# Kernel optimization log

Measured on AMD Instinct MI355X. Metric: run time of the kernel, lower is better.

The kernel has to match this reference:

```python
import jax, jax.numpy as jnp
import numpy as np

B, LQ, LK, D = 2, 2048, 2048, 1024
H, DK, DV = 16, 64, 64
EPS = 1e-6


def setup_inputs() -> dict:
    key = jax.random.key(0)
    ks = jax.random.split(key, 12)
    s = 1.0 / np.sqrt(D)
    return {
        "PE_states": jax.random.normal(ks[0], (B, LK, D), jnp.float32),
        "global_state": jax.random.normal(ks[1], (B, LQ, D), jnp.float32),
        "PE_statements": jax.random.normal(ks[2], (B, LK, D), jnp.float32),
        "PE_operators": jax.random.normal(ks[3], (B, LK, D), jnp.float32),
        "PE_solution_scores": jax.random.uniform(ks[4], (B, LK), jnp.float32),
        "mask": jax.random.randint(ks[5], (B, LQ, LK), 0, 2, jnp.int32),
        "w_q": jax.random.normal(ks[6], (D, H * DK), jnp.float32) * s,
        "w_k": jax.random.normal(ks[7], (D, H * DK), jnp.float32) * s,
        "w_v": jax.random.normal(ks[8], (D, H * DV), jnp.float32) * s,
        "w_fc": jax.random.normal(ks[9], (H * DV, D), jnp.float32) * s,
        "ln_gamma": jnp.ones((D,), jnp.float32),
        "ln_beta": jnp.zeros((D,), jnp.float32),
    }


def _layer_norm(x, gamma, beta):
    mu = jnp.mean(x, axis=-1, keepdims=True)
    var = jnp.mean(jnp.square(x - mu), axis=-1, keepdims=True)
    return (x - mu) * jax.lax.rsqrt(var + EPS) * gamma + beta


def reference(PE_states, global_state, PE_statements, PE_operators,
              PE_solution_scores, mask, w_q, w_k, w_v, w_fc, ln_gamma, ln_beta):
    # att_type == 'ca_sc', query_mode == 'PE', dropout == 0
    residual = global_state  # [B, LQ, D]
    q = (global_state @ w_q).reshape(B, LQ, H, DK).transpose(0, 2, 1, 3)   # bhqd
    k = (PE_states @ w_k).reshape(B, LK, H, DK).transpose(0, 2, 1, 3)      # bhkd
    v_s = (PE_statements @ w_v).reshape(B, LK, H, DV).transpose(0, 2, 1, 3)
    v_o = (PE_operators @ w_v).reshape(B, LK, H, DV).transpose(0, 2, 1, 3)

    temp = jnp.asarray(DK, jnp.float32) ** 0.5
    attn = jnp.einsum('bhqd,bhkd->bhqk', q / temp, k)  # [B,H,LQ,LK]
    # PE_solution_scores: per-key bias broadcast over heads and queries
    attn = (attn + PE_solution_scores[:, None, None, :]) / 2.0
    attn = jnp.where(mask[:, None, :, :] == 0, jnp.float32(-1e9), attn)
    attn = jax.nn.softmax(attn, axis=-1)

    def head_out(v):
        o = jnp.einsum('bhqk,bhkd->bhqd', attn, v)
        o = o.transpose(0, 2, 1, 3).reshape(B, LQ, H * DV)
        o = o @ w_fc + residual
        return _layer_norm(o, ln_gamma, ln_beta)

    statement_pred = head_out(v_s)
    operator_pred = head_out(v_o)
    return statement_pred, operator_pred
```

## Files before the change

### kernel.cpp

```cpp
#include <hip/hip_runtime.h>


typedef unsigned short u16;
typedef unsigned int   u32;
typedef unsigned long long u64;

typedef __attribute__((ext_vector_type(8))) short frag_ab;
typedef __attribute__((ext_vector_type(4))) float frag_cd;
typedef __attribute__((ext_vector_type(16))) float f32x16;
typedef __attribute__((ext_vector_type(8))) unsigned short u16x8;
typedef __attribute__((ext_vector_type(4))) unsigned short u16x4;
typedef __attribute__((ext_vector_type(2))) unsigned int u32x2;
typedef __attribute__((ext_vector_type(4))) int int4v;

__device__ __forceinline__ u16 f2bf(float f) {
    u32 x = __builtin_bit_cast(u32, f);
    return (u16)((x + 0x7fffu + ((x >> 16) & 1u)) >> 16);
}

__device__ __forceinline__ u32 pkbf(float a, float b) {
    return __builtin_amdgcn_perm(__builtin_bit_cast(u32, b),
                                 __builtin_bit_cast(u32, a), 0x07060302u);
}

#define GLDS16(gsrc, ldst)                                                     \
    __builtin_amdgcn_global_load_lds(                                          \
        (const __attribute__((address_space(1))) void*)(gsrc),                 \
        (__attribute__((address_space(3))) void*)(ldst), 16, 0, 0)

#define MFMA32(a, b, c) __builtin_amdgcn_mfma_f32_32x32x16_bf16(a, b, c, 0, 0, 0)

__global__ __launch_bounds__(256) void prep_kernel(
    const float* __restrict__ in0, const float* __restrict__ in1,
    const float* __restrict__ in2, const float* __restrict__ in3,
    u16* __restrict__ Ab4,
    const float* __restrict__ w_q, const float* __restrict__ w_k,
    const float* __restrict__ w_v, const float* __restrict__ w_fc,
    u16* __restrict__ wqT, u16* __restrict__ wkT,
    u16* __restrict__ wvT, u16* __restrict__ wfcT,
    const int* __restrict__ mask, u64* __restrict__ bits)
{
    __shared__ u16 tile[32][33];
    const int bid = blockIdx.x;
    const int tid = threadIdx.x;
    if (bid < 8192) {
        int z = bid >> 11;
        const float* in = z == 0 ? in0 : z == 1 ? in1 : z == 2 ? in2 : in3;
        u16* o = Ab4 + (size_t)z * 4194304;
        size_t i = ((size_t)(bid & 2047) * 256 + tid) * 8;
        float4 f0 = *(const float4*)(in + i);
        float4 f1 = *(const float4*)(in + i + 4);
        u16x8 t;
        t[0] = f2bf(f0.x); t[1] = f2bf(f0.y); t[2] = f2bf(f0.z); t[3] = f2bf(f0.w);
        t[4] = f2bf(f1.x); t[5] = f2bf(f1.y); t[6] = f2bf(f1.z); t[7] = f2bf(f1.w);
        *(u16x8*)(o + i) = t;
    } else if (bid < 12288) {
        int t = bid - 8192;
        int z = t >> 10;
        const float* in = z == 0 ? w_q : z == 1 ? w_k : z == 2 ? w_v : w_fc;
        u16* out = z == 0 ? wqT : z == 1 ? wkT : z == 2 ? wvT : wfcT;
        int bx = (t & 31) * 32, by = ((t >> 5) & 31) * 32;
        int tx = tid & 31, ty = tid >> 5;
        for (int i = 0; i < 32; i += 8)
            tile[ty + i][tx] = f2bf(in[(size_t)(by + ty + i) * 1024 + bx + tx]);
        __syncthreads();
        for (int i = 0; i < 32; i += 8)
            out[(size_t)(bx + ty + i) * 1024 + by + tx] = tile[tx][ty + i];
    } else {
        int pb = bid - 12288;
        int wv = tid >> 6, ln = tid & 63;
        long long base = (long long)pb * 2048 + wv * 512;
        for (int j = 0; j < 8; j++) {
            int v = mask[base + j * 64 + ln];
            u64 bl = __ballot(v != 0);
            if (ln == 0) bits[(base >> 6) + j] = bl;
        }
    }
}

__device__ __forceinline__ void gemm_core(
    const u16* __restrict__ A, const u16* __restrict__ BT,
    int bm, int bn, u16* Al, u16* Bl, frag_cd acc[4][4])
{
    const int tid = threadIdx.x;
    const int wave = tid >> 6, lane = tid & 63;
    const int ln15 = lane & 15, quad = lane >> 4;
    const int wm4 = (wave & 1) * 4, wn4 = (wave >> 1) * 4;

    for (int k0 = 0; k0 < 1024; k0 += 64) {
        for (int s = 0; s < 4; s++) {
            int f = wave * 4 + s;
            int grp = f >> 1, ks = f & 1;
            size_t col = k0 + ks * 32 + quad * 8;
            GLDS16(&A[(size_t)(bm + grp * 16 + ln15) * 1024 + col], Al + f * 512);
            GLDS16(&BT[(size_t)(bn + grp * 16 + ln15) * 1024 + col], Bl + f * 512);
        }
        __syncthreads();
        for (int ks = 0; ks < 2; ks++) {
            frag_ab a[4], b[4];
            for (int i = 0; i < 4; i++)
                a[i] = *(const frag_ab*)(Al + ((wm4 + i) * 2 + ks) * 512 + lane * 8);
            for (int j = 0; j < 4; j++)
                b[j] = *(const frag_ab*)(Bl + ((wn4 + j) * 2 + ks) * 512 + lane * 8);
            for (int i = 0; i < 4; i++)
                for (int j = 0; j < 4; j++)
                    acc[i][j] = __builtin_amdgcn_mfma_f32_16x16x32_bf16(a[i], b[j], acc[i][j], 0, 0, 0);
        }
        __syncthreads();
    }
}

__global__ __launch_bounds__(256, 3) void proj_gemm_kernel(
    const u16* __restrict__ Ab4,
    const u16* __restrict__ wqT, const u16* __restrict__ wkT, const u16* __restrict__ wvT,
    u16* __restrict__ Qb, u16* __restrict__ Kb,
    u16* __restrict__ VsT_g, u16* __restrict__ VoT_g)
{
    __shared__ alignas(16) u16 Al[16 * 512];
    __shared__ alignas(16) u16 Bl[16 * 512];
    const int z = blockIdx.z;
    const u16* A = Ab4 + (size_t)z * 4194304;
    const u16* BT = z == 0 ? wqT : z == 1 ? wkT : wvT;
    const int bm = blockIdx.x * 128, bn = blockIdx.y * 128;
    frag_cd acc[4][4] = {};
    gemm_core(A, BT, bm, bn, Al, Bl, acc);

    const int lane = threadIdx.x & 63;
    const int wave = threadIdx.x >> 6;
    const int ln15 = lane & 15, quad = lane >> 4;
    const int wm = (wave & 1) * 64, wn = (wave >> 1) * 64;
    if (z < 2) {
        u16* C = z == 0 ? Qb : Kb;
        const float qsc = z == 0 ? 0.09016844f : 1.0f;
        for (int i = 0; i < 4; i++) for (int j = 0; j < 4; j++) {
            int row0 = bm + wm + i * 16 + quad * 4;
            int col = bn + wn + j * 16 + ln15;
            for (int r = 0; r < 4; r++)
                C[(size_t)(row0 + r) * 1024 + col] = f2bf(acc[i][j][r] * qsc);
        }
    } else {
        u16* C = z == 2 ? VsT_g : VoT_g;
        for (int i = 0; i < 4; i++) for (int j = 0; j < 4; j++) {
            int row0 = bm + wm + i * 16 + quad * 4;
            int col = bn + wn + j * 16 + ln15;
            u16x4 t;
            for (int r = 0; r < 4; r++) t[r] = f2bf(acc[i][j][r]);
            *(u16x4*)&C[(size_t)col * 4096 + row0] = t;
        }
    }
}

__global__ __launch_bounds__(256, 3) void fc_gemm_kernel(
    const u16* __restrict__ Osb, const u16* __restrict__ Oob, const u16* __restrict__ wfcT,
    const float* __restrict__ resid, float* __restrict__ preLN)
{
    __shared__ alignas(16) u16 Al[16 * 512];
    __shared__ alignas(16) u16 Bl[16 * 512];
    const int z = blockIdx.z;
    const u16* A = z == 0 ? Osb : Oob;
    float* Cf = preLN + (size_t)z * 4194304;
    const int bm = blockIdx.x * 128, bn = blockIdx.y * 128;
    frag_cd acc[4][4] = {};
    gemm_core(A, wfcT, bm, bn, Al, Bl, acc);

    const int lane = threadIdx.x & 63;
    const int wave = threadIdx.x >> 6;
    const int ln15 = lane & 15, quad = lane >> 4;
    const int wm = (wave & 1) * 64, wn = (wave >> 1) * 64;
    for (int i = 0; i < 4; i++) for (int j = 0; j < 4; j++) {
        int row0 = bm + wm + i * 16 + quad * 4;
        int col = bn + wn + j * 16 + ln15;
        for (int r = 0; r < 4; r++) {
            size_t off = (size_t)(row0 + r) * 1024 + col;
            Cf[off] = acc[i][j][r] + resid[off];
        }
    }
}

__device__ __forceinline__ void flash_stage(
    const u16* __restrict__ Kp, const u16* __restrict__ VsT, const u16* __restrict__ VoT,
    int b, int h, int kt, int wave, int ln31, int hi, u16* buf)
{
    const int k0 = kt * 64;
    for (int s = 0; s < 6; s++) {
        int t = wave * 6 + s;
        const u16* g;
        if (t < 8) {
            int n = t >> 2, ks = t & 3;
            g = &Kp[(size_t)(b * 2048 + k0 + n * 32 + ln31) * 1024 + h * 64 + ks * 16 + hi * 8];
        } else if (t < 16) {
            int dt = (t >> 2) & 1, sk = t & 3;
            g = &VsT[(size_t)(h * 64 + dt * 32 + ln31) * 4096 + b * 2048 + k0 + sk * 16 + hi * 8];
        } else {
            int dt = (t >> 2) & 1, sk = t & 3;
            g = &VoT[(size_t)(h * 64 + dt * 32 + ln31) * 4096 + b * 2048 + k0 + sk * 16 + hi * 8];
        }
        GLDS16(g, buf + t * 512);
    }
}

__global__ __launch_bounds__(256, 2) void flash_kernel(
    const u16* __restrict__ Q, const u16* __restrict__ Kp,
    const u16* __restrict__ VsT_g, const u16* __restrict__ VoT_g,
    const float* __restrict__ scores, const u64* __restrict__ mbits,
    u16* __restrict__ Os, u16* __restrict__ Oo)
{
    __shared__ alignas(16) u16 KV[2][24 * 512];
    const int bid = blockIdx.x;
    const int xcd = bid & 7;
    const int qt = (bid >> 3) & 15;
    const int g = xcd + 8 * (bid >> 7);
    const int h = g & 15, b = g >> 4;
    const int tid = threadIdx.x;
    const int wave = tid >> 6, lane = tid & 63;
    const int ln31 = lane & 31, hi = lane >> 5;
    const int qbase = b * 2048 + qt * 128 + wave * 32;
    const int qrow = qbase + ln31;

    frag_ab aq0, aq1, aq2, aq3;
    {
        const u16* qp = &Q[(size_t)qrow * 1024 + h * 64 + hi * 8];
        aq0 = *(const frag_ab*)(qp);
        aq1 = *(const frag_ab*)(qp + 16);
        aq2 = *(const frag_ab*)(qp + 32);
        aq3 = *(const frag_ab*)(qp + 48);
    }
    frag_ab bbias = {};
    bbias[0] = (short)0x3F80; bbias[1] = (short)0x3F80;

    f32x16 os0 = {}, os1 = {}, oo0 = {}, oo1 = {};
    float l0 = 0.f, l1 = 0.f;
    const int shl4 = 4 - 4 * hi;

    auto softmax16 = [&](f32x16& s, u32 wa, float& lacc) {
#pragma unroll
        for (int r = 0; r < 16; r++) {
            const int bitc = (r & 3) + 8 * (r >> 2);
            u32 m = (u32)(((int)(wa << (27 - bitc))) >> 31);
            float e = __builtin_amdgcn_exp2f(s[r]);
            u32 pb = __builtin_bit_cast(u32, e) & m;
            float pf = __builtin_bit_cast(float, pb);
            lacc += pf;
            s[r] = pf;
        }
    };

    flash_stage(Kp, VsT_g, VoT_g, b, h, 0, wave, ln31, hi, KV[0]);

    for (int kt = 0; kt < 32; kt++) {
        const int p = kt & 1;
        float sc0f = scores[b * 2048 + kt * 64 + ln31];
        float sc1f = scores[b * 2048 + kt * 64 + 32 + ln31];
        u64 w = mbits[(size_t)qrow * 32 + kt];
        __syncthreads();
        if (kt < 31)
            flash_stage(Kp, VsT_g, VoT_g, b, h, kt + 1, wave, ln31, hi, KV[p ^ 1]);
        const u16* bufp = KV[p];

        frag_ab ab0 = {}, ab1 = {};
        if (!hi) {
            float t0 = sc0f * 0.72134752f;
            u16 c0 = f2bf(t0);
            ab0[0] = (short)c0;
            ab0[1] = (short)f2bf(t0 - __builtin_bit_cast(float, (u32)c0 << 16));
            float t1 = sc1f * 0.72134752f;
            u16 c1 = f2bf(t1);
            ab1[0] = (short)c1;
            ab1[1] = (short)f2bf(t1 - __builtin_bit_cast(float, (u32)c1 << 16));
        }

        f32x16 sacc0 = {}, sacc1 = {};
        sacc0 = MFMA32(ab0, bbias, sacc0);
        sacc1 = MFMA32(ab1, bbias, sacc1);
#pragma unroll
        for (int ks = 0; ks < 4; ks++) {
            frag_ab ak0 = *(const frag_ab*)(bufp + (0 * 4 + ks) * 512 + lane * 8);
            frag_ab ak1 = *(const frag_ab*)(bufp + (1 * 4 + ks) * 512 + lane * 8);
            frag_ab q = ks == 0 ? aq0 : ks == 1 ? aq1 : ks == 2 ? aq2 : aq3;
            sacc0 = MFMA32(ak0, q, sacc0);
            sacc1 = MFMA32(ak1, q, sacc1);
        }

        u32 wa0 = ((u32)w) << shl4;
        u32 wa1 = ((u32)(w >> 32)) << shl4;
        softmax16(sacc0, wa0, l0);
        softmax16(sacc1, wa1, l1);

#pragma unroll
        for (int sk = 0; sk < 4; sk++) {
            const f32x16& ps = (sk < 2) ? sacc0 : sacc1;
            const int e0 = (sk & 1) * 8;
            u32 a0 = pkbf(ps[e0 + 0], ps[e0 + 1]);
            u32 a1 = pkbf(ps[e0 + 2], ps[e0 + 3]);
            u32 b0 = pkbf(ps[e0 + 4], ps[e0 + 5]);
            u32 b1 = pkbf(ps[e0 + 6], ps[e0 + 7]);
            u32x2 r0 = __builtin_amdgcn_permlane32_swap(a0, b0, false, false);
            u32x2 r1 = __builtin_amdgcn_permlane32_swap(a1, b1, false, false);
            int4v iv;
            iv[0] = (int)r0[0]; iv[1] = (int)r1[0];
            iv[2] = (int)r0[1]; iv[3] = (int)r1[1];
            frag_ab ap = __builtin_bit_cast(frag_ab, iv);
            frag_ab bs0 = *(const frag_ab*)(bufp + (8 + sk) * 512 + lane * 8);
            frag_ab bs1 = *(const frag_ab*)(bufp + (12 + sk) * 512 + lane * 8);
            frag_ab bo0 = *(const frag_ab*)(bufp + (16 + sk) * 512 + lane * 8);
            frag_ab bo1 = *(const frag_ab*)(bufp + (20 + sk) * 512 + lane * 8);
            os0 = MFMA32(ap, bs0, os0);
            os1 = MFMA32(ap, bs1, os1);
            oo0 = MFMA32(ap, bo0, oo0);
            oo1 = MFMA32(ap, bo1, oo1);
        }
    }

    float l_run = l0 + l1;
    float l_tot = l_run + __shfl_xor(l_run, 32, 64);
#pragma unroll
    for (int r = 0; r < 16; r++) {
        const int qr = (r & 3) + 8 * (r >> 2) + 4 * hi;
        float lv = __shfl(l_tot, qr, 64);
        float inv = 1.0f / fmaxf(lv, 1e-30f);
        size_t row = (size_t)(qbase + qr) * 1024 + h * 64;
        Os[row + ln31]      = f2bf(os0[r] * inv);
        Os[row + 32 + ln31] = f2bf(os1[r] * inv);
        Oo[row + ln31]      = f2bf(oo0[r] * inv);
        Oo[row + 32 + ln31] = f2bf(oo1[r] * inv);
    }
}

__global__ __launch_bounds__(256) void ln_kernel(
    const float* __restrict__ X, const float* __restrict__ gamma, const float* __restrict__ beta,
    float* __restrict__ out)
{
    __shared__ float red[4];
    int row = blockIdx.x;
    int tid = threadIdx.x;
    const float* x = X + (size_t)row * 1024;
    float v[4];
    float s = 0.f;
    for (int i = 0; i < 4; i++) { v[i] = x[tid + i * 256]; s += v[i]; }
    for (int off = 1; off < 64; off <<= 1) s += __shfl_xor(s, off, 64);
    int wv = tid >> 6, ln = tid & 63;
    if (ln == 0) red[wv] = s;
    __syncthreads();
    float mean = (red[0] + red[1] + red[2] + red[3]) * (1.0f / 1024.0f);
    float s2 = 0.f;
    for (int i = 0; i < 4; i++) { float d = v[i] - mean; s2 += d * d; }
    for (int off = 1; off < 64; off <<= 1) s2 += __shfl_xor(s2, off, 64);
    __syncthreads();
    if (ln == 0) red[wv] = s2;
    __syncthreads();
    float var = (red[0] + red[1] + red[2] + red[3]) * (1.0f / 1024.0f);
    float rstd = rsqrtf(var + 1e-6f);
    for (int i = 0; i < 4; i++) {
        int c = tid + i * 256;
        out[(size_t)row * 1024 + c] = (v[i] - mean) * rstd * gamma[c] + beta[c];
    }
}

extern "C" void kernel_launch(void* const* d_in, const int* in_sizes, int n_in,
                              void* d_out, int out_size, void* d_ws, size_t ws_size,
                              hipStream_t stream)
{
    const float* PE_states     = (const float*)d_in[0];
    const float* global_state  = (const float*)d_in[1];
    const float* PE_statements = (const float*)d_in[2];
    const float* PE_operators  = (const float*)d_in[3];
    const float* scores        = (const float*)d_in[4];
    const int*   mask          = (const int*)d_in[5];
    const float* w_q  = (const float*)d_in[6];
    const float* w_k  = (const float*)d_in[7];
    const float* w_v  = (const float*)d_in[8];
    const float* w_fc = (const float*)d_in[9];
    const float* gamma = (const float*)d_in[10];
    const float* beta  = (const float*)d_in[11];
    float* out = (float*)d_out;

    char* ws = (char*)d_ws;
    const size_t MB = 1u << 20;
    u16* Ab4   = (u16*)(ws + 0 * MB);
    u16* Osb   = (u16*)(ws + 0 * MB);
    u16* Oob   = (u16*)(ws + 8 * MB);
    u16* wqT   = (u16*)(ws + 32 * MB);
    u16* wkT   = (u16*)(ws + 34 * MB);
    u16* wvT   = (u16*)(ws + 36 * MB);
    u16* wfcT  = (u16*)(ws + 38 * MB);
    u64* mbits = (u64*)(ws + 40 * MB);
    u16* Qb    = (u16*)(ws + 41 * MB);
    u16* Kb    = (u16*)(ws + 49 * MB);
    u16* VsT_g = (u16*)(ws + 57 * MB);
    u16* VoT_g = (u16*)(ws + 65 * MB);
    float* preLN = (float*)(ws + 41 * MB);

    prep_kernel<<<16384, 256, 0, stream>>>(
        global_state, PE_states, PE_statements, PE_operators, Ab4,
        w_q, w_k, w_v, w_fc, wqT, wkT, wvT, wfcT, mask, mbits);

    proj_gemm_kernel<<<dim3(32, 8, 4), 256, 0, stream>>>(
        Ab4, wqT, wkT, wvT, Qb, Kb, VsT_g, VoT_g);

    flash_kernel<<<dim3(512), 256, 0, stream>>>(Qb, Kb, VsT_g, VoT_g, scores, mbits, Osb, Oob);

    fc_gemm_kernel<<<dim3(32, 8, 2), 256, 0, stream>>>(Osb, Oob, wfcT, global_state, preLN);
    ln_kernel<<<8192, 256, 0, stream>>>(preLN, gamma, beta, out);
}
```

Baseline: 356.4 us.

## Triple-buffer flash K/V staging, vectorize layernorm, raise proj GEMM occupancy

The flash kernel moves from double to triple buffering of K/V tiles in LDS. Two tiles are prefetched ahead, and an explicit vmcnt wait plus a raw barrier replace __syncthreads, so the loads for tile kt+2 overlap compute on tile kt. The layernorm kernel now uses float4 loads and stores for x, gamma, beta and the output. The projection GEMM's launch bounds hint goes from 3 to 4 blocks per CU. The extra LDS buffer (72KB per block) may reduce flash occupancy, and the hand-written vmcnt(6) count depends on how many loads flash_stage issues per wave.

After: 359.3 us. Within noise of the previous version (+0.8%).

```diff
diff --git a/kernel.cpp b/kernel.cpp
--- a/kernel.cpp
+++ b/kernel.cpp
@@ -110,7 +110,7 @@
     }
 }
 
-__global__ __launch_bounds__(256, 3) void proj_gemm_kernel(
+__global__ __launch_bounds__(256, 4) void proj_gemm_kernel(
     const u16* __restrict__ Ab4,
     const u16* __restrict__ wqT, const u16* __restrict__ wkT, const u16* __restrict__ wvT,
     u16* __restrict__ Qb, u16* __restrict__ Kb,
@@ -205,7 +205,7 @@
     const float* __restrict__ scores, const u64* __restrict__ mbits,
     u16* __restrict__ Os, u16* __restrict__ Oo)
 {
-    __shared__ alignas(16) u16 KV[2][24 * 512];
+    __shared__ alignas(16) u16 KV[3][24 * 512];
     const int bid = blockIdx.x;
     const int xcd = bid & 7;
     const int qt = (bid >> 3) & 15;
@@ -246,16 +246,19 @@
     };
 
     flash_stage(Kp, VsT_g, VoT_g, b, h, 0, wave, ln31, hi, KV[0]);
+    flash_stage(Kp, VsT_g, VoT_g, b, h, 1, wave, ln31, hi, KV[1]);
 
     for (int kt = 0; kt < 32; kt++) {
-        const int p = kt & 1;
         float sc0f = scores[b * 2048 + kt * 64 + ln31];
         float sc1f = scores[b * 2048 + kt * 64 + 32 + ln31];
         u64 w = mbits[(size_t)qrow * 32 + kt];
-        __syncthreads();
-        if (kt < 31)
-            flash_stage(Kp, VsT_g, VoT_g, b, h, kt + 1, wave, ln31, hi, KV[p ^ 1]);
-        const u16* bufp = KV[p];
+        if (kt < 31) asm volatile("s_waitcnt vmcnt(6) lgkmcnt(0)" ::: "memory");
+        else         asm volatile("s_waitcnt vmcnt(0) lgkmcnt(0)" ::: "memory");
+        __builtin_amdgcn_s_barrier();
+        __builtin_amdgcn_sched_barrier(0);
+        if (kt < 30)
+            flash_stage(Kp, VsT_g, VoT_g, b, h, kt + 2, wave, ln31, hi, KV[(kt + 2) % 3]);
+        const u16* bufp = KV[kt % 3];
 
         frag_ab ab0 = {}, ab1 = {};
         if (!hi) {
@@ -334,26 +337,29 @@
     int row = blockIdx.x;
     int tid = threadIdx.x;
     const float* x = X + (size_t)row * 1024;
-    float v[4];
-    float s = 0.f;
-    for (int i = 0; i < 4; i++) { v[i] = x[tid + i * 256]; s += v[i]; }
+    float4 v = *(const float4*)(x + tid * 4);
+    float s = v.x + v.y + v.z + v.w;
     for (int off = 1; off < 64; off <<= 1) s += __shfl_xor(s, off, 64);
     int wv = tid >> 6, ln = tid & 63;
     if (ln == 0) red[wv] = s;
     __syncthreads();
     float mean = (red[0] + red[1] + red[2] + red[3]) * (1.0f / 1024.0f);
-    float s2 = 0.f;
-    for (int i = 0; i < 4; i++) { float d = v[i] - mean; s2 += d * d; }
+    float dx = v.x - mean, dy = v.y - mean, dz = v.z - mean, dw = v.w - mean;
+    float s2 = dx * dx + dy * dy + dz * dz + dw * dw;
     for (int off = 1; off < 64; off <<= 1) s2 += __shfl_xor(s2, off, 64);
     __syncthreads();
     if (ln == 0) red[wv] = s2;
     __syncthreads();
     float var = (red[0] + red[1] + red[2] + red[3]) * (1.0f / 1024.0f);
     float rstd = rsqrtf(var + 1e-6f);
-    for (int i = 0; i < 4; i++) {
-        int c = tid + i * 256;
-        out[(size_t)row * 1024 + c] = (v[i] - mean) * rstd * gamma[c] + beta[c];
-    }
+    float4 gg = *(const float4*)(gamma + tid * 4);
+    float4 bb = *(const float4*)(beta + tid * 4);
+    float4 o;
+    o.x = dx * rstd * gg.x + bb.x;
+    o.y = dy * rstd * gg.y + bb.y;
+    o.z = dz * rstd * gg.z + bb.z;
+    o.w = dw * rstd * gg.w + bb.w;
+    *(float4*)(out + (size_t)row * 1024 + tid * 4) = o;
 }
 
 extern "C" void kernel_launch(void* const* d_in, const int* in_sizes, int n_in,
```
